# Kernel tuning notes

Measured on AMD Instinct MI355X. Metric: run time of the kernel, lower is better.

Reference implementation:

```python
import jax, jax.numpy as jnp
import numpy as np

B, T, U = 256, 2048, 512

def setup_inputs() -> dict:
    key = jax.random.key(0)
    kx, kw = jax.random.split(key)
    x = jax.random.normal(kx, (B, T, U), dtype=jnp.float32)
    W = jax.random.normal(kw, (U, 1), dtype=jnp.float32) * (1.0 / np.sqrt(U))
    b = jnp.zeros((T, 1), dtype=jnp.float32)
    return {"x": x, "W": W, "b": b}

def reference(x, W, b):
    # e: (B, T, 1) scalar score per timestep
    e = jnp.tanh(jnp.einsum('btu,uo->bto', x, W) + b)
    # softmax over time axis
    a = jax.nn.softmax(e, axis=1)
    # weighted sum over T -> (B, U)
    return jnp.sum(x * a, axis=1)
```

## Files before the change

### kernel.cpp

```cpp
#include <hip/hip_runtime.h>
#include <cstdint>


#define NW    16
#define BLOCK (NW * 64)
#define UDIM  512

__global__ __launch_bounds__(BLOCK, 1)
void attn_pool_fused(const float* __restrict__ x,
                     const float* __restrict__ Wv,
                     const float* __restrict__ bv,
                     float* __restrict__ out, int T) {
    const int bidx = blockIdx.x;
    const int tid  = threadIdx.x;
    const int w    = tid >> 6;
    const int lane = tid & 63;
    const int u0   = lane << 3;

    const float4* wp  = (const float4*)(Wv + u0);
    const float4  wA  = wp[0];
    const float4  wB  = wp[1];

    const float* xb = x + (size_t)bidx * (size_t)T * UDIM;

    float m = -1.0f, l = 0.0f;
    float o0=0.f,o1=0.f,o2=0.f,o3=0.f,o4=0.f,o5=0.f,o6=0.f,o7=0.f;

    int t = w;
    const float4* p0 = (const float4*)(xb + (size_t)t * UDIM + u0);
    float4 c0 = p0[0];
    float4 c1 = p0[1];

    const int iters = T / NW;
    for (int i = 0; i < iters; ++i) {
        int tn = t + NW;
        int tf = (tn < T) ? tn : t;
        const float4* pn = (const float4*)(xb + (size_t)tf * UDIM + u0);
        float4 n0 = pn[0];
        float4 n1 = pn[1];

        float d = c0.x*wA.x + c0.y*wA.y + c0.z*wA.z + c0.w*wA.w
                + c1.x*wB.x + c1.y*wB.y + c1.z*wB.z + c1.w*wB.w;
        #pragma unroll
        for (int off = 32; off >= 1; off >>= 1)
            d += __shfl_xor(d, off, 64);

        float s  = d + bv[t];
        float ex = __expf(2.0f * s);
        float e  = (ex - 1.0f) / (ex + 1.0f);

        float mn = fmaxf(m, e);
        float sc = __expf(m - mn);
        float pr = __expf(e - mn);
        l  = l * sc + pr;
        o0 = o0 * sc + pr * c0.x;
        o1 = o1 * sc + pr * c0.y;
        o2 = o2 * sc + pr * c0.z;
        o3 = o3 * sc + pr * c0.w;
        o4 = o4 * sc + pr * c1.x;
        o5 = o5 * sc + pr * c1.y;
        o6 = o6 * sc + pr * c1.z;
        o7 = o7 * sc + pr * c1.w;
        m = mn;

        c0 = n0; c1 = n1;
        t = tn;
    }

    __shared__ float sm_m[NW];
    __shared__ float sm_l[NW];
    __shared__ float sm_o[NW][UDIM];
    if (lane == 0) { sm_m[w] = m; sm_l[w] = l; }
    float4* so = (float4*)&sm_o[w][u0];
    so[0] = make_float4(o0, o1, o2, o3);
    so[1] = make_float4(o4, o5, o6, o7);
    __syncthreads();

    if (tid < UDIM) {
        float M = -1.0f;
        #pragma unroll
        for (int j = 0; j < NW; ++j) M = fmaxf(M, sm_m[j]);
        float L = 0.0f, acc = 0.0f;
        #pragma unroll
        for (int j = 0; j < NW; ++j) {
            float s = __expf(sm_m[j] - M);
            L   += s * sm_l[j];
            acc += s * sm_o[j][tid];
        }
        out[(size_t)bidx * UDIM + tid] = acc / L;
    }
}

extern "C" void kernel_launch(void* const* d_in, const int* in_sizes, int n_in,
                              void* d_out, int out_size, void* d_ws, size_t ws_size,
                              hipStream_t stream) {
    const float* x  = (const float*)d_in[0];
    const float* W  = (const float*)d_in[1];
    const float* bb = (const float*)d_in[2];
    float* out      = (float*)d_out;

    const int U = in_sizes[1];
    const int T = in_sizes[2];
    const int B = in_sizes[0] / (T * U);
    (void)U; (void)n_in; (void)out_size; (void)d_ws; (void)ws_size;

    attn_pool_fused<<<B, BLOCK, 0, stream>>>(x, W, bb, out, T);
}
```

Measured before the change: 1.309 ms.

## Process four timesteps per wave with DPP reductions and deeper prefetch

Each wave now handles a contiguous group of four timesteps per iteration and prefetches the next group of four rows. This raises memory-level parallelism and amortizes the online-softmax rescale across four steps. The shuffle-based wave reduction is replaced with DPP row operations plus readlane, and tanh uses a hardware reciprocal. The costs are more registers per thread and a float4 load of bias that assumes alignment.

```diff
diff --git a/kernel.cpp b/kernel.cpp
--- a/kernel.cpp
+++ b/kernel.cpp
@@ -5,6 +5,30 @@
 #define NW    16
 #define BLOCK (NW * 64)
 #define UDIM  512
+#define RG    4
+#define TSTEP (NW * RG)
+
+__device__ __forceinline__ float dpp_sum64(float x) {
+    int t;
+    t = __builtin_amdgcn_update_dpp(0, __float_as_int(x), 0x111, 0xf, 0xf, true); x += __int_as_float(t);
+    t = __builtin_amdgcn_update_dpp(0, __float_as_int(x), 0x112, 0xf, 0xf, true); x += __int_as_float(t);
+    t = __builtin_amdgcn_update_dpp(0, __float_as_int(x), 0x114, 0xf, 0xf, true); x += __int_as_float(t);
+    t = __builtin_amdgcn_update_dpp(0, __float_as_int(x), 0x118, 0xf, 0xf, true); x += __int_as_float(t);
+    t = __builtin_amdgcn_update_dpp(0, __float_as_int(x), 0x142, 0xa, 0xf, true); x += __int_as_float(t);
+    t = __builtin_amdgcn_update_dpp(0, __float_as_int(x), 0x143, 0xc, 0xf, true); x += __int_as_float(t);
+    return __int_as_float(__builtin_amdgcn_readlane(__float_as_int(x), 63));
+}
+
+__device__ __forceinline__ float dot4(float4 a, float4 b) {
+    return fmaf(a.x, b.x, fmaf(a.y, b.y, fmaf(a.z, b.z, a.w * b.w)));
+}
+__device__ __forceinline__ float4 f4fma(float s, float4 a, float4 c) {
+    return make_float4(fmaf(s, a.x, c.x), fmaf(s, a.y, c.y),
+                       fmaf(s, a.z, c.z), fmaf(s, a.w, c.w));
+}
+__device__ __forceinline__ float4 f4scale(float4 a, float s) {
+    return make_float4(a.x * s, a.y * s, a.z * s, a.w * s);
+}
 
 __global__ __launch_bounds__(BLOCK, 1)
 void attn_pool_fused(const float* __restrict__ x,
@@ -17,54 +41,82 @@
     const int lane = tid & 63;
     const int u0   = lane << 3;
 
-    const float4* wp  = (const float4*)(Wv + u0);
-    const float4  wA  = wp[0];
-    const float4  wB  = wp[1];
+    const float4* wp = (const float4*)(Wv + u0);
+    const float4  wA = wp[0];
+    const float4  wB = wp[1];
 
     const float* xb = x + (size_t)bidx * (size_t)T * UDIM;
 
-    float m = -1.0f, l = 0.0f;
-    float o0=0.f,o1=0.f,o2=0.f,o3=0.f,o4=0.f,o5=0.f,o6=0.f,o7=0.f;
+    float  m = -1.0f, l = 0.0f;
+    float4 oA = make_float4(0.f, 0.f, 0.f, 0.f);
+    float4 oB = make_float4(0.f, 0.f, 0.f, 0.f);
 
-    int t = w;
-    const float4* p0 = (const float4*)(xb + (size_t)t * UDIM + u0);
-    float4 c0 = p0[0];
-    float4 c1 = p0[1];
+    float4 cc[RG][2], nn[RG][2];
 
-    const int iters = T / NW;
+    int tb = w * RG;
+    {
+        const float* p = xb + (size_t)tb * UDIM + u0;
+        #pragma unroll
+        for (int r = 0; r < RG; ++r) {
+            cc[r][0] = ((const float4*)p)[0];
+            cc[r][1] = ((const float4*)p)[1];
+            p += UDIM;
+        }
+    }
+
+    const int iters = T / TSTEP;
     for (int i = 0; i < iters; ++i) {
-        int tn = t + NW;
-        int tf = (tn < T) ? tn : t;
-        const float4* pn = (const float4*)(xb + (size_t)tf * UDIM + u0);
-        float4 n0 = pn[0];
-        float4 n1 = pn[1];
+        const int tn = tb + TSTEP;
+        const int tf = (i + 1 < iters) ? tn : tb;
+        {
+            const float* p = xb + (size_t)tf * UDIM + u0;
+            #pragma unroll
+            for (int r = 0; r < RG; ++r) {
+                nn[r][0] = ((const float4*)p)[0];
+                nn[r][1] = ((const float4*)p)[1];
+                p += UDIM;
+            }
+        }
 
-        float d = c0.x*wA.x + c0.y*wA.y + c0.z*wA.z + c0.w*wA.w
-                + c1.x*wB.x + c1.y*wB.y + c1.z*wB.z + c1.w*wB.w;
-        #pragma unroll
-        for (int off = 32; off >= 1; off >>= 1)
-            d += __shfl_xor(d, off, 64);
+        const float4 bvv = *(const float4*)(bv + tb);
 
-        float s  = d + bv[t];
-        float ex = __expf(2.0f * s);
-        float e  = (ex - 1.0f) / (ex + 1.0f);
+        float d0 = dot4(cc[0][0], wA) + dot4(cc[0][1], wB);
+        float d1 = dot4(cc[1][0], wA) + dot4(cc[1][1], wB);
+        float d2 = dot4(cc[2][0], wA) + dot4(cc[2][1], wB);
+        float d3 = dot4(cc[3][0], wA) + dot4(cc[3][1], wB);
+        d0 = dpp_sum64(d0);
+        d1 = dpp_sum64(d1);
+        d2 = dpp_sum64(d2);
+        d3 = dpp_sum64(d3);
 
-        float mn = fmaxf(m, e);
-        float sc = __expf(m - mn);
-        float pr = __expf(e - mn);
-        l  = l * sc + pr;
-        o0 = o0 * sc + pr * c0.x;
-        o1 = o1 * sc + pr * c0.y;
-        o2 = o2 * sc + pr * c0.z;
-        o3 = o3 * sc + pr * c0.w;
-        o4 = o4 * sc + pr * c1.x;
-        o5 = o5 * sc + pr * c1.y;
-        o6 = o6 * sc + pr * c1.z;
-        o7 = o7 * sc + pr * c1.w;
+        float s0 = d0 + bvv.x, s1 = d1 + bvv.y, s2 = d2 + bvv.z, s3 = d3 + bvv.w;
+        float e0 = 1.0f - 2.0f * __builtin_amdgcn_rcpf(__expf(2.0f * s0) + 1.0f);
+        float e1 = 1.0f - 2.0f * __builtin_amdgcn_rcpf(__expf(2.0f * s1) + 1.0f);
+        float e2 = 1.0f - 2.0f * __builtin_amdgcn_rcpf(__expf(2.0f * s2) + 1.0f);
+        float e3 = 1.0f - 2.0f * __builtin_amdgcn_rcpf(__expf(2.0f * s3) + 1.0f);
+
+        const float gm = fmaxf(fmaxf(e0, e1), fmaxf(e2, e3));
+        const float mn = fmaxf(m, gm);
+        const float sc = __expf(m - mn);
+        const float p0 = __expf(e0 - mn);
+        const float p1 = __expf(e1 - mn);
+        const float p2 = __expf(e2 - mn);
+        const float p3 = __expf(e3 - mn);
+        l = fmaf(l, sc, (p0 + p1) + (p2 + p3));
+        oA = f4scale(oA, sc);
+        oB = f4scale(oB, sc);
+        oA = f4fma(p0, cc[0][0], oA);  oB = f4fma(p0, cc[0][1], oB);
+        oA = f4fma(p1, cc[1][0], oA);  oB = f4fma(p1, cc[1][1], oB);
+        oA = f4fma(p2, cc[2][0], oA);  oB = f4fma(p2, cc[2][1], oB);
+        oA = f4fma(p3, cc[3][0], oA);  oB = f4fma(p3, cc[3][1], oB);
         m = mn;
 
-        c0 = n0; c1 = n1;
-        t = tn;
+        #pragma unroll
+        for (int r = 0; r < RG; ++r) {
+            cc[r][0] = nn[r][0];
+            cc[r][1] = nn[r][1];
+        }
+        tb = tn;
     }
 
     __shared__ float sm_m[NW];
@@ -72,8 +124,8 @@
     __shared__ float sm_o[NW][UDIM];
     if (lane == 0) { sm_m[w] = m; sm_l[w] = l; }
     float4* so = (float4*)&sm_o[w][u0];
-    so[0] = make_float4(o0, o1, o2, o3);
-    so[1] = make_float4(o4, o5, o6, o7);
+    so[0] = oA;
+    so[1] = oB;
     __syncthreads();
 
     if (tid < UDIM) {
```

Result: no change. 1.316 ms (+0.5%).
